# Kernel optimization log

Measured on AMD Instinct MI355X. Metric: run time of the kernel, lower is better.

Reference implementation:

```python
import jax, jax.numpy as jnp
import numpy as np
import math

IN_DIM = 256
OUT_DIM = 256
HEADS = 4
D_K = OUT_DIM // HEADS


def setup_inputs() -> dict:
    key = jax.random.key(0)
    ks = jax.random.split(key, 10)
    B, N = 4, 4096
    x = jax.random.normal(ks[0], (B, N, IN_DIM), dtype=jnp.float32)
    adj = jax.random.randint(ks[1], (B, N, N), 0, 2, dtype=jnp.int32)
    s = 1.0 / math.sqrt(IN_DIM)
    Wq = jax.random.normal(ks[2], (IN_DIM, OUT_DIM), dtype=jnp.float32) * s
    bq = jnp.zeros((OUT_DIM,), dtype=jnp.float32)
    Wk = jax.random.normal(ks[3], (IN_DIM, OUT_DIM), dtype=jnp.float32) * s
    bk = jnp.zeros((OUT_DIM,), dtype=jnp.float32)
    Wv = jax.random.normal(ks[4], (IN_DIM, OUT_DIM), dtype=jnp.float32) * s
    bv = jnp.zeros((OUT_DIM,), dtype=jnp.float32)
    Wo = jax.random.normal(ks[5], (OUT_DIM, OUT_DIM), dtype=jnp.float32) * (1.0 / math.sqrt(OUT_DIM))
    bo = jnp.zeros((OUT_DIM,), dtype=jnp.float32)
    return {"x": x, "adj": adj, "Wq": Wq, "bq": bq, "Wk": Wk, "bk": bk,
            "Wv": Wv, "bv": bv, "Wo": Wo, "bo": bo}


def reference(x, adj, Wq, bq, Wk, bk, Wv, bv, Wo, bo):
    B, N, _ = x.shape
    q = (x @ Wq + bq).reshape(B, N, HEADS, D_K)
    k = (x @ Wk + bk).reshape(B, N, HEADS, D_K)
    v = (x @ Wv + bv).reshape(B, N, HEADS, D_K)
    scale = 1.0 / math.sqrt(D_K + 1e-9)
    scores = jnp.einsum('bnhd,bmhd->bhnm', q, k) * scale  # [B,H,N,N]
    eye = jnp.eye(N, dtype=bool)
    mask = (adj.astype(bool) | eye)[:, None, :, :]  # [B,1,N,N]
    min_val = jnp.finfo(scores.dtype).min
    scores = jnp.where(mask, scores, min_val)
    attn = jax.nn.softmax(scores, axis=-1)
    out = jnp.einsum('bhnm,bmhd->bnhd', attn, v).reshape(B, N, OUT_DIM)
    out = out @ Wo + bo
    return jax.nn.relu(out)
```

## Files before the change

kernel.cpp:

```cpp
#include <hip/hip_runtime.h>
#include <hip/hip_bf16.h>

#define DI 256
#define DOUT 256
#define NH 4
#define NB 4
#define NN 4096

typedef __attribute__((ext_vector_type(8))) short bf16x8;
typedef __attribute__((ext_vector_type(4))) float f32x4;
typedef __attribute__((ext_vector_type(4))) unsigned short u16x4;

#define MFMA16(a, b, c) __builtin_amdgcn_mfma_f32_16x16x32_bf16((a), (b), (c), 0, 0, 0)

#define SCALE_L2E 0.18033688011112043f
#define DEFER_THR 8.0f

static __device__ __forceinline__ unsigned short f2bf(float f) {
  union { __hip_bfloat16 h; unsigned short u; } c;
  c.h = __float2bfloat16(f);
  return c.u;
}

__global__ __launch_bounds__(256) void k_cvt_x(const float* __restrict__ x,
                                               unsigned short* __restrict__ xb) {
  int i = blockIdx.x * 256 + threadIdx.x;
  float4 v = ((const float4*)x)[i];
  u16x4 o;
  o[0] = f2bf(v.x); o[1] = f2bf(v.y); o[2] = f2bf(v.z); o[3] = f2bf(v.w);
  ((u16x4*)xb)[i] = o;
}

__global__ __launch_bounds__(256) void k_cvt_w(
    const float* __restrict__ Wq, const float* __restrict__ Wk,
    const float* __restrict__ Wv, const float* __restrict__ Wo,
    unsigned short* __restrict__ wtq, unsigned short* __restrict__ wtk,
    unsigned short* __restrict__ wtv, unsigned short* __restrict__ wto) {
  int t = blockIdx.x * 256 + threadIdx.x;
  int k = t >> 8, n = t & 255;
  int d = n * 256 + k;
  wtq[d] = f2bf(Wq[t]);
  wtk[d] = f2bf(Wk[t]);
  wtv[d] = f2bf(Wv[t]);
  wto[d] = f2bf(Wo[t]);
}

__global__ __launch_bounds__(256) void k_proj(
    const unsigned short* __restrict__ xb,
    const unsigned short* __restrict__ wtq, const unsigned short* __restrict__ wtk,
    const unsigned short* __restrict__ wtv,
    const float* __restrict__ bq, const float* __restrict__ bk, const float* __restrict__ bv,
    unsigned short* __restrict__ qh, unsigned short* __restrict__ kh,
    unsigned short* __restrict__ vtb) {
  const int tid = threadIdx.x, w = tid >> 6, l = tid & 63, ql = l & 15, g = l >> 4;
  const int wz = blockIdx.z;
  const unsigned short* wt = (wz == 0) ? wtq : (wz == 1 ? wtk : wtv);
  const float* bias = (wz == 0) ? bq : (wz == 1 ? bk : bv);
  const int node0 = blockIdx.x * 64, nout0 = blockIdx.y * 64;
  const int wn = w >> 1, wm = w & 1;

  const unsigned short* a0 = wt + (size_t)(nout0 + 32 * wn + ql) * 256 + g * 8;
  const unsigned short* b0 = xb + (size_t)(node0 + 32 * wm + ql) * 256 + g * 8;

  f32x4 acc[2][2] = {};
#pragma unroll
  for (int kk = 0; kk < 256; kk += 32) {
    bf16x8 af0 = *(const bf16x8*)(a0 + kk);
    bf16x8 af1 = *(const bf16x8*)(a0 + 16 * 256 + kk);
    bf16x8 bf0 = *(const bf16x8*)(b0 + kk);
    bf16x8 bf1 = *(const bf16x8*)(b0 + 16 * 256 + kk);
    acc[0][0] = MFMA16(af0, bf0, acc[0][0]);
    acc[0][1] = MFMA16(af0, bf1, acc[0][1]);
    acc[1][0] = MFMA16(af1, bf0, acc[1][0]);
    acc[1][1] = MFMA16(af1, bf1, acc[1][1]);
  }
  const int h = blockIdx.y;
  const float sc = (wz == 0) ? SCALE_L2E : 1.0f;
#pragma unroll
  for (int tn = 0; tn < 2; ++tn) {
    const int d0 = 32 * wn + 16 * tn + 4 * g;
    float bi[4];
#pragma unroll
    for (int r = 0; r < 4; ++r) bi[r] = bias[nout0 + d0 + r];
#pragma unroll
    for (int tm = 0; tm < 2; ++tm) {
      const int node = node0 + 32 * wm + 16 * tm + ql;
      const int b = node >> 12, n = node & 4095;
      if (wz < 2) {
        unsigned short* dst = (wz == 0 ? qh : kh) +
            ((size_t)(b * NH + h) * NN + n) * 64 + d0;
        u16x4 pk;
#pragma unroll
        for (int r = 0; r < 4; ++r) pk[r] = f2bf((acc[tn][tm][r] + bi[r]) * sc);
        *(u16x4*)dst = pk;
      } else {
#pragma unroll
        for (int r = 0; r < 4; ++r) {
          vtb[((size_t)(b * NH + h) * 64 + d0 + r) * NN + n] =
              f2bf(acc[tn][tm][r] + bi[r]);
        }
      }
    }
  }
}

__global__ __launch_bounds__(256, 2) void k_attn(
    const unsigned short* __restrict__ qh, const unsigned short* __restrict__ kh,
    const unsigned short* __restrict__ vtb, const int* __restrict__ adj,
    unsigned short* __restrict__ aout) {
  const int tid = threadIdx.x, w = tid >> 6, l = tid & 63, ql = l & 15, g = l >> 4;
  const int b = blockIdx.y, n0 = blockIdx.x * 32, h = w;
  const unsigned short* qbase = qh + ((size_t)(b * NH + h) * NN + n0) * 64;
  const unsigned short* kbase = kh + (size_t)(b * NH + h) * NN * 64;
  const unsigned short* vbase = vtb + (size_t)(b * NH + h) * 64 * NN;
  const int* adjb = adj + ((size_t)b * NN + n0) * NN;

  bf16x8 qf[2][2];
#pragma unroll
  for (int qt = 0; qt < 2; ++qt) {
    qf[qt][0] = *(const bf16x8*)(qbase + (size_t)(16 * qt + ql) * 64 + g * 8);
    qf[qt][1] = *(const bf16x8*)(qbase + (size_t)(16 * qt + ql) * 64 + 32 + g * 8);
  }

  __shared__ unsigned long long lmask[2][32];
  __shared__ unsigned short plds[4][16][72];

  float mrun[2] = {-1e30f, -1e30f}, lrun[2] = {0.f, 0.f};
  f32x4 oacc[2][4] = {};

#pragma unroll
  for (int j = 0; j < 8; ++j) {
    const int row = 8 * w + j;
    int a = adjb[(size_t)row * NN + l];
    unsigned long long bal = __ballot(a != 0);
    if (l == 0) lmask[0][row] = bal;
  }
  __syncthreads();

  for (int t0 = 0; t0 < NN; t0 += 64) {
    const int buf = (t0 >> 6) & 1;
    int anext[8];
    const bool more = (t0 + 64) < NN;
    if (more) {
#pragma unroll
      for (int j = 0; j < 8; ++j)
        anext[j] = adjb[(size_t)(8 * w + j) * NN + (t0 + 64) + l];
    }
    f32x4 s[2][4];
#pragma unroll
    for (int t = 0; t < 4; ++t) {
      const unsigned short* kr = kbase + (size_t)(t0 + 16 * t + ql) * 64 + g * 8;
      bf16x8 kf0 = *(const bf16x8*)kr;
      bf16x8 kf1 = *(const bf16x8*)(kr + 32);
#pragma unroll
      for (int qt = 0; qt < 2; ++qt) {
        f32x4 z = {};
        z = MFMA16(kf0, qf[qt][0], z);
        s[qt][t] = MFMA16(kf1, qf[qt][1], z);
      }
    }
    if (more) {
#pragma unroll
      for (int j = 0; j < 8; ++j) {
        unsigned long long bal = __ballot(anext[j] != 0);
        if (l == 0) lmask[buf ^ 1][8 * w + j] = bal;
      }
    }

    bf16x8 vf[4][2];
#pragma unroll
    for (int qt = 0; qt < 2; ++qt) {
      const int nq = n0 + 16 * qt + ql;
      unsigned long long rm = lmask[buf][16 * qt + ql];
      const int dg = nq - t0;
      if (dg >= 0 && dg < 64) rm |= (1ull << dg);
      float sv[16];
      float mx = -__builtin_inff();
#pragma unroll
      for (int t = 0; t < 4; ++t)
#pragma unroll
        for (int r = 0; r < 4; ++r) {
          const int idx = 16 * t + 4 * g + r;
          float vvv = ((rm >> idx) & 1ull) ? s[qt][t][r] : -__builtin_inff();
          sv[4 * t + r] = vvv;
          mx = fmaxf(mx, vvv);
        }
      mx = fmaxf(mx, __shfl_xor(mx, 16));
      mx = fmaxf(mx, __shfl_xor(mx, 32));
      if (!__all(mx <= mrun[qt] + DEFER_THR)) {
        const float mnew = fmaxf(mrun[qt], mx);
        const float fsc = exp2f(mrun[qt] - mnew);
        lrun[qt] *= fsc;
#pragma unroll
        for (int u = 0; u < 4; ++u)
#pragma unroll
          for (int r = 0; r < 4; ++r) oacc[qt][u][r] *= fsc;
        mrun[qt] = mnew;
      }
      float ls = 0.f;
      unsigned short pb[16];
#pragma unroll
      for (int i = 0; i < 16; ++i) {
        float p = exp2f(sv[i] - mrun[qt]);
        ls += p;
        pb[i] = f2bf(p);
      }
      ls += __shfl_xor(ls, 16);
      ls += __shfl_xor(ls, 32);
      lrun[qt] += ls;
      unsigned short* prow = &plds[w][ql][0];
#pragma unroll
      for (int t = 0; t < 4; ++t) {
        u16x4 pk;
        pk[0] = pb[4 * t]; pk[1] = pb[4 * t + 1];
        pk[2] = pb[4 * t + 2]; pk[3] = pb[4 * t + 3];
        *(u16x4*)(prow + 16 * t + 4 * g) = pk;
      }
      bf16x8 pf0 = *(const bf16x8*)(prow + g * 8);
      bf16x8 pf1 = *(const bf16x8*)(prow + 32 + g * 8);
#pragma unroll
      for (int u = 0; u < 4; ++u) {
        if (qt == 0) {
          const unsigned short* vr = vbase + (size_t)(16 * u + ql) * NN + t0 + g * 8;
          vf[u][0] = *(const bf16x8*)vr;
          vf[u][1] = *(const bf16x8*)(vr + 32);
        }
        oacc[qt][u] = MFMA16(vf[u][0], pf0, oacc[qt][u]);
        oacc[qt][u] = MFMA16(vf[u][1], pf1, oacc[qt][u]);
      }
    }
    __syncthreads();
  }

#pragma unroll
  for (int qt = 0; qt < 2; ++qt) {
    const int nq = n0 + 16 * qt + ql;
    const float inv = 1.f / lrun[qt];
    unsigned short* obase = aout + ((size_t)b * NN + nq) * DOUT + h * 64;
#pragma unroll
    for (int u = 0; u < 4; ++u) {
      u16x4 pk;
#pragma unroll
      for (int r = 0; r < 4; ++r) pk[r] = f2bf(oacc[qt][u][r] * inv);
      *(u16x4*)(obase + 16 * u + 4 * g) = pk;
    }
  }
}

__global__ __launch_bounds__(256) void k_oproj(
    const unsigned short* __restrict__ aout, const unsigned short* __restrict__ wto,
    const float* __restrict__ bo, float* __restrict__ out) {
  const int tid = threadIdx.x, w = tid >> 6, l = tid & 63, ql = l & 15, g = l >> 4;
  const int node0 = blockIdx.x * 64, nout0 = blockIdx.y * 64;
  const int wm = w & 1, wn = w >> 1;
  const unsigned short* a0 = aout + (size_t)(node0 + 32 * wm + ql) * 256 + g * 8;
  const unsigned short* b0 = wto + (size_t)(nout0 + 32 * wn + ql) * 256 + g * 8;

  f32x4 acc[2][2] = {};
#pragma unroll
  for (int kk = 0; kk < 256; kk += 32) {
    bf16x8 af0 = *(const bf16x8*)(a0 + kk);
    bf16x8 af1 = *(const bf16x8*)(a0 + 16 * 256 + kk);
    bf16x8 bf0 = *(const bf16x8*)(b0 + kk);
    bf16x8 bf1 = *(const bf16x8*)(b0 + 16 * 256 + kk);
    acc[0][0] = MFMA16(af0, bf0, acc[0][0]);
    acc[0][1] = MFMA16(af0, bf1, acc[0][1]);
    acc[1][0] = MFMA16(af1, bf0, acc[1][0]);
    acc[1][1] = MFMA16(af1, bf1, acc[1][1]);
  }
  float bi[2];
  bi[0] = bo[nout0 + 32 * wn + ql];
  bi[1] = bo[nout0 + 32 * wn + 16 + ql];
#pragma unroll
  for (int tm = 0; tm < 2; ++tm) {
    const int nodeb = node0 + 32 * wm + 16 * tm + 4 * g;
#pragma unroll
    for (int tn = 0; tn < 2; ++tn) {
      const int nout = nout0 + 32 * wn + 16 * tn + ql;
#pragma unroll
      for (int r = 0; r < 4; ++r) {
        float v = acc[tm][tn][r] + bi[tn];
        out[(size_t)(nodeb + r) * 256 + nout] = fmaxf(v, 0.f);
      }
    }
  }
}

extern "C" void kernel_launch(void* const* d_in, const int* in_sizes, int n_in,
                              void* d_out, int out_size, void* d_ws, size_t ws_size,
                              hipStream_t stream) {
  const float* x  = (const float*)d_in[0];
  const int*   adj = (const int*)d_in[1];
  const float* Wq = (const float*)d_in[2];
  const float* bq = (const float*)d_in[3];
  const float* Wk = (const float*)d_in[4];
  const float* bk = (const float*)d_in[5];
  const float* Wv = (const float*)d_in[6];
  const float* bv = (const float*)d_in[7];
  const float* Wo = (const float*)d_in[8];
  const float* bo = (const float*)d_in[9];
  float* out = (float*)d_out;

  unsigned short* ws = (unsigned short*)d_ws;
  const size_t NX = (size_t)NB * NN * DI;
  unsigned short* xb  = ws;
  unsigned short* wtq = xb + NX;
  unsigned short* wtk = wtq + 65536;
  unsigned short* wtv = wtk + 65536;
  unsigned short* wto = wtv + 65536;
  unsigned short* qhb = wto + 65536;
  unsigned short* khb = qhb + NX;
  unsigned short* vtb = khb + NX;
  unsigned short* aout = xb;

  k_cvt_x<<<(int)(NX / 4 / 256), 256, 0, stream>>>(x, xb);
  k_cvt_w<<<256, 256, 0, stream>>>(Wq, Wk, Wv, Wo, wtq, wtk, wtv, wto);
  dim3 gp(NB * NN / 64, 4, 3);
  k_proj<<<gp, 256, 0, stream>>>(xb, wtq, wtk, wtv, bq, bk, bv, qhb, khb, vtb);
  dim3 ga(NN / 32, NB);
  k_attn<<<ga, 256, 0, stream>>>(qhb, khb, vtb, adj, aout);
  dim3 go(NB * NN / 64, 4);
  k_oproj<<<go, 256, 0, stream>>>(aout, wto, bo, out);
}
```

Before: 688.8 us.

## Prepack adjacency bitmask and stage K/V tiles into LDS asynchronously

Adds a separate kernel that packs the int32 adjacency into 64-bit bitmasks, stored in the output buffer as scratch, so the attention kernel reads masks instead of raw int32 rows. Attention is reorganised so each block handles one head and 64 queries. K and V tiles are double-buffered into swizzled LDS with global_load_lds, and the kernel now targets 4 blocks per CU. The weight conversion is also vectorised. The adjacency must still be read once, but the packing pass adds a launch, and reusing the output buffer relies on it being overwritten later.

```diff
diff --git a/kernel.cpp b/kernel.cpp
--- a/kernel.cpp
+++ b/kernel.cpp
@@ -10,6 +10,7 @@
 typedef __attribute__((ext_vector_type(8))) short bf16x8;
 typedef __attribute__((ext_vector_type(4))) float f32x4;
 typedef __attribute__((ext_vector_type(4))) unsigned short u16x4;
+typedef __attribute__((ext_vector_type(8))) unsigned short u16x8;
 
 #define MFMA16(a, b, c) __builtin_amdgcn_mfma_f32_16x16x32_bf16((a), (b), (c), 0, 0, 0)
 
@@ -20,6 +21,12 @@
   union { __hip_bfloat16 h; unsigned short u; } c;
   c.h = __float2bfloat16(f);
   return c.u;
+}
+
+static __device__ __forceinline__ void gl_lds16(const void* g, void* l) {
+  __builtin_amdgcn_global_load_lds(
+      (const __attribute__((address_space(1))) void*)g,
+      (__attribute__((address_space(3))) void*)l, 16, 0, 0);
 }
 
 __global__ __launch_bounds__(256) void k_cvt_x(const float* __restrict__ x,
@@ -37,12 +44,28 @@
     unsigned short* __restrict__ wtq, unsigned short* __restrict__ wtk,
     unsigned short* __restrict__ wtv, unsigned short* __restrict__ wto) {
   int t = blockIdx.x * 256 + threadIdx.x;
-  int k = t >> 8, n = t & 255;
-  int d = n * 256 + k;
-  wtq[d] = f2bf(Wq[t]);
-  wtk[d] = f2bf(Wk[t]);
-  wtv[d] = f2bf(Wv[t]);
-  wto[d] = f2bf(Wo[t]);
+  int m = t >> 13, k0 = ((t >> 8) & 31) * 8, n = t & 255;
+  const float* W = (m == 0) ? Wq : (m == 1) ? Wk : (m == 2) ? Wv : Wo;
+  unsigned short* dst = (m == 0) ? wtq : (m == 1) ? wtk : (m == 2) ? wtv : wto;
+  u16x8 o;
+#pragma unroll
+  for (int j = 0; j < 8; ++j) o[j] = f2bf(W[(k0 + j) * 256 + n]);
+  *(u16x8*)(dst + n * 256 + k0) = o;
+}
+
+__global__ __launch_bounds__(256) void k_pack(const int* __restrict__ adj,
+                                              unsigned long long* __restrict__ pm) {
+  const int gw = blockIdx.x * 4 + (threadIdx.x >> 6);
+  const int l = threadIdx.x & 63;
+  const int b = gw >> 15, c = (gw >> 9) & 63, n0 = (gw & 511) << 3;
+  unsigned long long myb = 0;
+#pragma unroll
+  for (int j = 0; j < 8; ++j) {
+    int a = adj[((size_t)b * NN + n0 + j) * NN + c * 64 + l];
+    unsigned long long bal = __ballot(a != 0);
+    if (l == j) myb = bal;
+  }
+  if (l < 8) pm[((size_t)b * 64 + c) * NN + n0 + l] = myb;
 }
 
 __global__ __launch_bounds__(256) void k_proj(
@@ -104,146 +127,136 @@
   }
 }
 
-__global__ __launch_bounds__(256, 2) void k_attn(
+__global__ __launch_bounds__(256, 4) void k_attn(
     const unsigned short* __restrict__ qh, const unsigned short* __restrict__ kh,
-    const unsigned short* __restrict__ vtb, const int* __restrict__ adj,
+    const unsigned short* __restrict__ vtb, const unsigned long long* __restrict__ pm,
     unsigned short* __restrict__ aout) {
   const int tid = threadIdx.x, w = tid >> 6, l = tid & 63, ql = l & 15, g = l >> 4;
-  const int b = blockIdx.y, n0 = blockIdx.x * 32, h = w;
-  const unsigned short* qbase = qh + ((size_t)(b * NH + h) * NN + n0) * 64;
-  const unsigned short* kbase = kh + (size_t)(b * NH + h) * NN * 64;
-  const unsigned short* vbase = vtb + (size_t)(b * NH + h) * 64 * NN;
-  const int* adjb = adj + ((size_t)b * NN + n0) * NN;
-
-  bf16x8 qf[2][2];
-#pragma unroll
-  for (int qt = 0; qt < 2; ++qt) {
-    qf[qt][0] = *(const bf16x8*)(qbase + (size_t)(16 * qt + ql) * 64 + g * 8);
-    qf[qt][1] = *(const bf16x8*)(qbase + (size_t)(16 * qt + ql) * 64 + 32 + g * 8);
-  }
-
-  __shared__ unsigned long long lmask[2][32];
-  __shared__ unsigned short plds[4][16][72];
-
-  float mrun[2] = {-1e30f, -1e30f}, lrun[2] = {0.f, 0.f};
-  f32x4 oacc[2][4] = {};
-
-#pragma unroll
-  for (int j = 0; j < 8; ++j) {
-    const int row = 8 * w + j;
-    int a = adjb[(size_t)row * NN + l];
-    unsigned long long bal = __ballot(a != 0);
-    if (l == 0) lmask[0][row] = bal;
-  }
+  const int n0 = blockIdx.x * 64, b = blockIdx.y, h = blockIdx.z;
+  const int nq = n0 + 16 * w + ql;
+
+  const unsigned short* qbase = qh + ((size_t)(b * NH + h) * NN + n0 + 16 * w) * 64;
+  const char* kg = (const char*)(kh + (size_t)(b * NH + h) * NN * 64);
+  const char* vg = (const char*)(vtb + (size_t)(b * NH + h) * 64 * NN);
+  const unsigned long long* pmrow = pm + (size_t)b * 64 * NN + nq;
+
+  __shared__ __align__(16) unsigned short kst[2][4096];
+  __shared__ __align__(16) unsigned short vst[2][4096];
+  __shared__ __align__(16) unsigned short plds[4][1024];
+
+  bf16x8 qf0 = *(const bf16x8*)(qbase + ql * 64 + g * 8);
+  bf16x8 qf1 = *(const bf16x8*)(qbase + ql * 64 + 32 + g * 8);
+
+  const int swzc = ((l & 7) << 4) ^ ((l >> 3) << 4);
+  const int lk = ((l >> 3) << 7) + swzc;
+  const int lv = (l >> 3) * (NN * 2) + swzc;
+  const int i0 = 2 * w, i1 = 2 * w + 1;
+  char* klds = (char*)kst;
+  char* vlds = (char*)vst;
+
+#define STAGE(B, T)                                                              \
+  do {                                                                           \
+    gl_lds16(kg + (size_t)(T) * 8192 + i0 * 1024 + lk, klds + (B) * 8192 + i0 * 1024); \
+    gl_lds16(kg + (size_t)(T) * 8192 + i1 * 1024 + lk, klds + (B) * 8192 + i1 * 1024); \
+    gl_lds16(vg + (size_t)(T) * 128 + (size_t)i0 * (8 * NN * 2) + lv,            \
+             vlds + (B) * 8192 + i0 * 1024);                                     \
+    gl_lds16(vg + (size_t)(T) * 128 + (size_t)i1 * (8 * NN * 2) + lv,            \
+             vlds + (B) * 8192 + i1 * 1024);                                     \
+  } while (0)
+
+  float mrun = -1e30f, lrun = 0.f;
+  f32x4 oacc[4] = {};
+  const int swz = (ql & 7) << 4;
+  char* prow = (char*)&plds[w][0] + ql * 128;
+
+  STAGE(0, 0);
+  unsigned long long rm_cur = pmrow[0];
+  unsigned long long rm_next = 0;
   __syncthreads();
 
-  for (int t0 = 0; t0 < NN; t0 += 64) {
-    const int buf = (t0 >> 6) & 1;
-    int anext[8];
-    const bool more = (t0 + 64) < NN;
-    if (more) {
-#pragma unroll
-      for (int j = 0; j < 8; ++j)
-        anext[j] = adjb[(size_t)(8 * w + j) * NN + (t0 + 64) + l];
-    }
-    f32x4 s[2][4];
-#pragma unroll
-    for (int t = 0; t < 4; ++t) {
-      const unsigned short* kr = kbase + (size_t)(t0 + 16 * t + ql) * 64 + g * 8;
-      bf16x8 kf0 = *(const bf16x8*)kr;
-      bf16x8 kf1 = *(const bf16x8*)(kr + 32);
-#pragma unroll
-      for (int qt = 0; qt < 2; ++qt) {
-        f32x4 z = {};
-        z = MFMA16(kf0, qf[qt][0], z);
-        s[qt][t] = MFMA16(kf1, qf[qt][1], z);
+  int buf = 0;
+  for (int t = 0; t < NN / 64; ++t) {
+    if (t < NN / 64 - 1) {
+      STAGE(buf ^ 1, t + 1);
+      rm_next = pmrow[(size_t)(t + 1) * NN];
+    }
+    f32x4 s[4];
+    const char* kb = klds + buf * 8192;
+#pragma unroll
+    for (int t4 = 0; t4 < 4; ++t4) {
+      const char* kr = kb + (16 * t4 + ql) * 128;
+      bf16x8 kf0 = *(const bf16x8*)(kr + ((g * 16) ^ swz));
+      bf16x8 kf1 = *(const bf16x8*)(kr + ((64 + g * 16) ^ swz));
+      f32x4 z = {};
+      z = MFMA16(kf0, qf0, z);
+      s[t4] = MFMA16(kf1, qf1, z);
+    }
+    unsigned long long rm = rm_cur;
+    const int dg = nq - (t << 6);
+    if (dg >= 0 && dg < 64) rm |= (1ull << dg);
+    float sv[16];
+    float mx = -__builtin_inff();
+#pragma unroll
+    for (int t4 = 0; t4 < 4; ++t4)
+#pragma unroll
+      for (int r = 0; r < 4; ++r) {
+        const int idx = 16 * t4 + 4 * g + r;
+        float vv = ((rm >> idx) & 1ull) ? s[t4][r] : -__builtin_inff();
+        sv[4 * t4 + r] = vv;
+        mx = fmaxf(mx, vv);
       }
-    }
-    if (more) {
-#pragma unroll
-      for (int j = 0; j < 8; ++j) {
-        unsigned long long bal = __ballot(anext[j] != 0);
-        if (l == 0) lmask[buf ^ 1][8 * w + j] = bal;
+    mx = fmaxf(mx, __shfl_xor(mx, 16));
+    mx = fmaxf(mx, __shfl_xor(mx, 32));
+    if (!__all(mx <= mrun + DEFER_THR)) {
+      const float mnew = fmaxf(mrun, mx);
+      const float fsc = exp2f(mrun - mnew);
+      lrun *= fsc;
+#pragma unroll
+      for (int u = 0; u < 4; ++u)
+#pragma unroll
+        for (int r = 0; r < 4; ++r) oacc[u][r] *= fsc;
+      mrun = mnew;
+    }
+    float ls = 0.f;
+#pragma unroll
+    for (int t4 = 0; t4 < 4; ++t4) {
+      u16x4 pk;
+#pragma unroll
+      for (int r = 0; r < 4; ++r) {
+        float p = exp2f(sv[4 * t4 + r] - mrun);
+        ls += p;
+        pk[r] = f2bf(p);
       }
-    }
-
-    bf16x8 vf[4][2];
-#pragma unroll
-    for (int qt = 0; qt < 2; ++qt) {
-      const int nq = n0 + 16 * qt + ql;
-      unsigned long long rm = lmask[buf][16 * qt + ql];
-      const int dg = nq - t0;
-      if (dg >= 0 && dg < 64) rm |= (1ull << dg);
-      float sv[16];
-      float mx = -__builtin_inff();
-#pragma unroll
-      for (int t = 0; t < 4; ++t)
-#pragma unroll
-        for (int r = 0; r < 4; ++r) {
-          const int idx = 16 * t + 4 * g + r;
-          float vvv = ((rm >> idx) & 1ull) ? s[qt][t][r] : -__builtin_inff();
-          sv[4 * t + r] = vvv;
-          mx = fmaxf(mx, vvv);
-        }
-      mx = fmaxf(mx, __shfl_xor(mx, 16));
-      mx = fmaxf(mx, __shfl_xor(mx, 32));
-      if (!__all(mx <= mrun[qt] + DEFER_THR)) {
-        const float mnew = fmaxf(mrun[qt], mx);
-        const float fsc = exp2f(mrun[qt] - mnew);
-        lrun[qt] *= fsc;
-#pragma unroll
-        for (int u = 0; u < 4; ++u)
-#pragma unroll
-          for (int r = 0; r < 4; ++r) oacc[qt][u][r] *= fsc;
-        mrun[qt] = mnew;
-      }
-      float ls = 0.f;
-      unsigned short pb[16];
-#pragma unroll
-      for (int i = 0; i < 16; ++i) {
-        float p = exp2f(sv[i] - mrun[qt]);
-        ls += p;
-        pb[i] = f2bf(p);
-      }
-      ls += __shfl_xor(ls, 16);
-      ls += __shfl_xor(ls, 32);
-      lrun[qt] += ls;
-      unsigned short* prow = &plds[w][ql][0];
-#pragma unroll
-      for (int t = 0; t < 4; ++t) {
-        u16x4 pk;
-        pk[0] = pb[4 * t]; pk[1] = pb[4 * t + 1];
-        pk[2] = pb[4 * t + 2]; pk[3] = pb[4 * t + 3];
-        *(u16x4*)(prow + 16 * t + 4 * g) = pk;
-      }
-      bf16x8 pf0 = *(const bf16x8*)(prow + g * 8);
-      bf16x8 pf1 = *(const bf16x8*)(prow + 32 + g * 8);
-#pragma unroll
-      for (int u = 0; u < 4; ++u) {
-        if (qt == 0) {
-          const unsigned short* vr = vbase + (size_t)(16 * u + ql) * NN + t0 + g * 8;
-          vf[u][0] = *(const bf16x8*)vr;
-          vf[u][1] = *(const bf16x8*)(vr + 32);
-        }
-        oacc[qt][u] = MFMA16(vf[u][0], pf0, oacc[qt][u]);
-        oacc[qt][u] = MFMA16(vf[u][1], pf1, oacc[qt][u]);
-      }
+      *(u16x4*)(prow + ((32 * t4 + 8 * g) ^ swz)) = pk;
+    }
+    ls += __shfl_xor(ls, 16);
+    ls += __shfl_xor(ls, 32);
+    lrun += ls;
+    bf16x8 pf0 = *(const bf16x8*)(prow + ((g * 16) ^ swz));
+    bf16x8 pf1 = *(const bf16x8*)(prow + ((64 + g * 16) ^ swz));
+    const char* vb = vlds + buf * 8192;
+#pragma unroll
+    for (int u = 0; u < 4; ++u) {
+      const char* vr = vb + (16 * u + ql) * 128;
+      bf16x8 vf0 = *(const bf16x8*)(vr + ((g * 16) ^ swz));
+      bf16x8 vf1 = *(const bf16x8*)(vr + ((64 + g * 16) ^ swz));
+      oacc[u] = MFMA16(vf0, pf0, oacc[u]);
+      oacc[u] = MFMA16(vf1, pf1, oacc[u]);
     }
     __syncthreads();
-  }
-
-#pragma unroll
-  for (int qt = 0; qt < 2; ++qt) {
-    const int nq = n0 + 16 * qt + ql;
-    const float inv = 1.f / lrun[qt];
-    unsigned short* obase = aout + ((size_t)b * NN + nq) * DOUT + h * 64;
-#pragma unroll
-    for (int u = 0; u < 4; ++u) {
-      u16x4 pk;
-#pragma unroll
-      for (int r = 0; r < 4; ++r) pk[r] = f2bf(oacc[qt][u][r] * inv);
-      *(u16x4*)(obase + 16 * u + 4 * g) = pk;
-    }
+    buf ^= 1;
+    rm_cur = rm_next;
+  }
+#undef STAGE
+
+  const float inv = 1.f / lrun;
+  unsigned short* obase = aout + ((size_t)b * NN + nq) * DOUT + h * 64;
+#pragma unroll
+  for (int u = 0; u < 4; ++u) {
+    u16x4 pk;
+#pragma unroll
+    for (int r = 0; r < 4; ++r) pk[r] = f2bf(oacc[u][r] * inv);
+    *(u16x4*)(obase + 16 * u + 4 * g) = pk;
   }
 }
 
@@ -312,13 +325,15 @@
   unsigned short* khb = qhb + NX;
   unsigned short* vtb = khb + NX;
   unsigned short* aout = xb;
+  unsigned long long* pmask = (unsigned long long*)d_out;
 
   k_cvt_x<<<(int)(NX / 4 / 256), 256, 0, stream>>>(x, xb);
-  k_cvt_w<<<256, 256, 0, stream>>>(Wq, Wk, Wv, Wo, wtq, wtk, wtv, wto);
+  k_cvt_w<<<128, 256, 0, stream>>>(Wq, Wk, Wv, Wo, wtq, wtk, wtv, wto);
+  k_pack<<<32768, 256, 0, stream>>>(adj, pmask);
   dim3 gp(NB * NN / 64, 4, 3);
   k_proj<<<gp, 256, 0, stream>>>(xb, wtq, wtk, wtv, bq, bk, bv, qhb, khb, vtb);
-  dim3 ga(NN / 32, NB);
-  k_attn<<<ga, 256, 0, stream>>>(qhb, khb, vtb, adj, aout);
+  dim3 ga(NN / 64, NB, NH);
+  k_attn<<<ga, 256, 0, stream>>>(qhb, khb, vtb, pmask, aout);
   dim3 go(NB * NN / 64, 4);
   k_oproj<<<go, 256, 0, stream>>>(aout, wto, bo, out);
 }
```

New measurement: 618.5 us. -10.2%, faster.
